# Kernel optimization log

Hardware: AMD Instinct MI355X
Metric: run time of the kernel (lower is better)

Reference implementation:

```python
import jax, jax.numpy as jnp
import numpy as np
import math

D = 3  # feature dim hardcoded in source


def setup_inputs() -> dict:
    key = jax.random.key(0)
    k1, k2, k3, k4 = jax.random.split(key, 4)
    B, H, S = 4, 8, 2048
    x = jax.random.normal(k1, (B, 1, S, D), dtype=jnp.float32)
    W_query = jax.random.normal(k2, (1, H, D, D), dtype=jnp.float32)
    W_key = jax.random.uniform(k3, (1, H, D, D), dtype=jnp.float32)
    W_value = jax.random.uniform(k4, (1, H, D, D), dtype=jnp.float32)
    return {"x": x, "W_query": W_query, "W_key": W_key, "W_value": W_value}


def reference(x, W_query, W_key, W_value):
    # Q/K/V projections: [B,1,S,d] @ [1,H,d,d] -> [B,H,S,d]
    Q = jnp.einsum('bosd,ohde->bhse', x, W_query)
    K = jnp.einsum('bosd,ohde->bhse', x, W_key)
    V = jnp.einsum('bosd,ohde->bhse', x, W_value)
    scale = 1.0 / math.sqrt(D)
    # scores: [B,H,S,S]
    scores = jnp.einsum('bhqd,bhkd->bhqk', Q, K) * scale
    weights = jax.nn.softmax(scores, axis=-1)
    ctx = jnp.einsum('bhqk,bhkd->bhqd', weights, V)
    # source returns (torch result, flash result) — mathematically identical
    return (ctx, ctx)
```

## Files before the change

### kernel.cpp

```cpp
#include <hip/hip_runtime.h>

#define SEQ 2048
#define NH 8
#define NB 4

typedef unsigned int u32;
typedef short bf16x8_t __attribute__((ext_vector_type(8)));
typedef float f32x16_t __attribute__((ext_vector_type(16)));

__device__ __forceinline__ u32 pkb(float a, float b) {
    const u32 ua = __builtin_bit_cast(u32, a) + 0x8000u;
    const u32 ub = __builtin_bit_cast(u32, b) + 0x8000u;
    return __builtin_amdgcn_perm(ub, ua, 0x07060302u);
}
__device__ __forceinline__ u32 pks(float Fa, float Fb) {
    return __builtin_amdgcn_perm(__builtin_bit_cast(u32, Fb),
                                 __builtin_bit_cast(u32, Fa), 0x05040100u);
}

union UBv { bf16x8_t v; u32 u[4]; };

__global__ __launch_bounds__(512)
void attn_mfma(const float* __restrict__ x, const float* __restrict__ Wq,
               const float* __restrict__ Wk, const float* __restrict__ Wv,
               float* __restrict__ out) {
    __shared__ __align__(16) char VT4[128 * 128];
    __shared__ __align__(16) float RED[4][8][8][16];

    const int tid = threadIdx.x;
    const int blk = blockIdx.x;
    const int qb   = blk & 63;
    const int rest = blk >> 6;
    const int hp   = rest & 1;
    const int b    = rest >> 1;
    const int hbase = hp * 4;

    const float* xb = x + b * SEQ * 3;

    const int lane = tid & 63;
    const int wid  = tid >> 6;
    const int ql   = lane & 31;
    const int q    = qb * 32 + ql;
    const int kbase = wid * 256;

    float ax0[8], ax1[8], ax2[8];
#pragma unroll
    for (int t = 0; t < 8; ++t) {
        const float* kp = xb + (kbase + t * 32 + ql) * 3;
        ax0[t] = kp[0]; ax1[t] = kp[1]; ax2[t] = kp[2];
    }

    {
        const float4* xg = (const float4*)xb;
        float xv[12];
        const float4 t0 = xg[tid * 3 + 0]; xv[0]=t0.x; xv[1]=t0.y; xv[2]=t0.z; xv[3]=t0.w;
        const float4 t1 = xg[tid * 3 + 1]; xv[4]=t1.x; xv[5]=t1.y; xv[6]=t1.z; xv[7]=t1.w;
        const float4 t2 = xg[tid * 3 + 2]; xv[8]=t2.x; xv[9]=t2.y; xv[10]=t2.z; xv[11]=t2.w;
        const int k0   = tid * 4;
        const int kt   = k0 >> 4;
        const int run  = k0 & 12;
        const int slotA = (run & 3) | ((run & 4) << 1) | ((run & 8) >> 1);
        char* base = VT4 + kt * 128;
#pragma unroll
        for (int d = 0; d < 3; ++d) {
            uint2 wa;
            wa.x = pkb(xv[0 + d], xv[3 + d]);
            wa.y = pkb(xv[6 + d], xv[9 + d]);
            *(uint2*)(base + d * 32 + slotA * 2) = wa;
        }
        uint2 ones; ones.x = ones.y = 0x3F803F80u;
        *(uint2*)(base + 96 + (k0 & 15) * 2) = ones;
    }

    u32 A0[8], A1h[4];
#pragma unroll
    for (int t = 0; t < 8; ++t) A0[t] = pkb(ax0[t], ax1[t]);
#pragma unroll
    for (int j = 0; j < 4; ++j) A1h[j] = pkb(ax2[2 * j], ax2[2 * j + 1]);

    const float* gq = xb + q * 3;
    const float xq0 = gq[0], xq1 = gq[1], xq2 = gq[2];
    const float cc = 0.5773502691896258f * 1.4426950408889634f * 128.0f;
    float uu[4][3];
#pragma unroll
    for (int hh = 0; hh < 4; ++hh) {
        const float* wqp = Wq + (hbase + hh) * 9;
        const float* wkp = Wk + (hbase + hh) * 9;
        const float Q0 = xq0 * wqp[0] + xq1 * wqp[3] + xq2 * wqp[6];
        const float Q1 = xq0 * wqp[1] + xq1 * wqp[4] + xq2 * wqp[7];
        const float Q2 = xq0 * wqp[2] + xq1 * wqp[5] + xq2 * wqp[8];
        uu[hh][0] = (Q0 * wkp[0] + Q1 * wkp[1] + Q2 * wkp[2]) * cc;
        uu[hh][1] = (Q0 * wkp[3] + Q1 * wkp[4] + Q2 * wkp[5]) * cc;
        uu[hh][2] = (Q0 * wkp[6] + Q1 * wkp[7] + Q2 * wkp[8]) * cc;
    }

    __syncthreads();

    UBv Bs0, Bs1, Bs2, Bs3;
    Bs0.u[0] = (lane < 32) ? pkb(uu[0][0], uu[0][1]) : 0u;
    Bs0.u[1] = (lane < 32) ? pkb(uu[0][2], 0.f) : 0u;
    Bs0.u[2] = 0u; Bs0.u[3] = 0u;
    Bs1.u[0] = (lane < 32) ? pkb(uu[1][0], uu[1][1]) : 0u;
    Bs1.u[1] = (lane < 32) ? pkb(uu[1][2], 0.f) : 0u;
    Bs1.u[2] = 0u; Bs1.u[3] = 0u;
    Bs2.u[0] = (lane < 32) ? pkb(uu[2][0], uu[2][1]) : 0u;
    Bs2.u[1] = (lane < 32) ? pkb(uu[2][2], 0.f) : 0u;
    Bs2.u[2] = 0u; Bs2.u[3] = 0u;
    Bs3.u[0] = (lane < 32) ? pkb(uu[3][0], uu[3][1]) : 0u;
    Bs3.u[1] = (lane < 32) ? pkb(uu[3][2], 0.f) : 0u;
    Bs3.u[2] = 0u; Bs3.u[3] = 0u;

    const char* vb = VT4 + wid * 2048 + (lane & 3) * 32 + (lane >> 5) * 16;

    f32x16_t bc;
#pragma unroll
    for (int i = 0; i < 16; ++i) bc[i] = 8404864.0f;

    const int d31 = lane & 31;
    const int slot = ((lane >> 5) << 2) | d31;

    f32x16_t pv0 = {}, pv1 = {}, pv2 = {}, pv3 = {};

#pragma unroll
    for (int t = 0; t < 8; ++t) {
        const uint4 bv0 = *(const uint4*)(vb + t * 256);
        const uint4 bv1 = *(const uint4*)(vb + t * 256 + 128);
        UBv B0; B0.u[0] = bv0.x; B0.u[1] = bv0.y; B0.u[2] = bv0.z; B0.u[3] = bv0.w;
        UBv B1; B1.u[0] = bv1.x; B1.u[1] = bv1.y; B1.u[2] = bv1.z; B1.u[3] = bv1.w;

        UBv A;
        A.u[0] = A0[t];
        A.u[1] = (t & 1) ? (A1h[t >> 1] >> 16) : (A1h[t >> 1] & 0xFFFFu);
        A.u[2] = 0u; A.u[3] = 0u;

        {
            const f32x16_t sc = __builtin_amdgcn_mfma_f32_32x32x16_bf16(A.v, Bs0.v, bc, 0, 0, 0);
            UBv PA;
            PA.u[0] = pks(sc[0],  sc[1]);  PA.u[1] = pks(sc[2],  sc[3]);
            PA.u[2] = pks(sc[4],  sc[5]);  PA.u[3] = pks(sc[6],  sc[7]);
            pv0 = __builtin_amdgcn_mfma_f32_32x32x16_bf16(PA.v, B0.v, pv0, 0, 0, 0);
            UBv PB;
            PB.u[0] = pks(sc[8],  sc[9]);  PB.u[1] = pks(sc[10], sc[11]);
            PB.u[2] = pks(sc[12], sc[13]); PB.u[3] = pks(sc[14], sc[15]);
            pv0 = __builtin_amdgcn_mfma_f32_32x32x16_bf16(PB.v, B1.v, pv0, 0, 0, 0);
        }
        {
            const f32x16_t sc = __builtin_amdgcn_mfma_f32_32x32x16_bf16(A.v, Bs1.v, bc, 0, 0, 0);
            UBv PA;
            PA.u[0] = pks(sc[0],  sc[1]);  PA.u[1] = pks(sc[2],  sc[3]);
            PA.u[2] = pks(sc[4],  sc[5]);  PA.u[3] = pks(sc[6],  sc[7]);
            pv1 = __builtin_amdgcn_mfma_f32_32x32x16_bf16(PA.v, B0.v, pv1, 0, 0, 0);
            UBv PB;
            PB.u[0] = pks(sc[8],  sc[9]);  PB.u[1] = pks(sc[10], sc[11]);
            PB.u[2] = pks(sc[12], sc[13]); PB.u[3] = pks(sc[14], sc[15]);
            pv1 = __builtin_amdgcn_mfma_f32_32x32x16_bf16(PB.v, B1.v, pv1, 0, 0, 0);
        }
        {
            const f32x16_t sc = __builtin_amdgcn_mfma_f32_32x32x16_bf16(A.v, Bs2.v, bc, 0, 0, 0);
            UBv PA;
            PA.u[0] = pks(sc[0],  sc[1]);  PA.u[1] = pks(sc[2],  sc[3]);
            PA.u[2] = pks(sc[4],  sc[5]);  PA.u[3] = pks(sc[6],  sc[7]);
            pv2 = __builtin_amdgcn_mfma_f32_32x32x16_bf16(PA.v, B0.v, pv2, 0, 0, 0);
            UBv PB;
            PB.u[0] = pks(sc[8],  sc[9]);  PB.u[1] = pks(sc[10], sc[11]);
            PB.u[2] = pks(sc[12], sc[13]); PB.u[3] = pks(sc[14], sc[15]);
            pv2 = __builtin_amdgcn_mfma_f32_32x32x16_bf16(PB.v, B1.v, pv2, 0, 0, 0);
        }
        {
            const f32x16_t sc = __builtin_amdgcn_mfma_f32_32x32x16_bf16(A.v, Bs3.v, bc, 0, 0, 0);
            UBv PA;
            PA.u[0] = pks(sc[0],  sc[1]);  PA.u[1] = pks(sc[2],  sc[3]);
            PA.u[2] = pks(sc[4],  sc[5]);  PA.u[3] = pks(sc[6],  sc[7]);
            pv3 = __builtin_amdgcn_mfma_f32_32x32x16_bf16(PA.v, B0.v, pv3, 0, 0, 0);
            UBv PB;
            PB.u[0] = pks(sc[8],  sc[9]);  PB.u[1] = pks(sc[10], sc[11]);
            PB.u[2] = pks(sc[12], sc[13]); PB.u[3] = pks(sc[14], sc[15]);
            pv3 = __builtin_amdgcn_mfma_f32_32x32x16_bf16(PB.v, B1.v, pv3, 0, 0, 0);
        }
    }

    if (d31 < 4) {
#pragma unroll
        for (int i = 0; i < 4; ++i) {
            float4 w;
            w.x = pv0[i*4+0]; w.y = pv0[i*4+1]; w.z = pv0[i*4+2]; w.w = pv0[i*4+3];
            *(float4*)&RED[0][wid][slot][i * 4] = w;
            w.x = pv1[i*4+0]; w.y = pv1[i*4+1]; w.z = pv1[i*4+2]; w.w = pv1[i*4+3];
            *(float4*)&RED[1][wid][slot][i * 4] = w;
            w.x = pv2[i*4+0]; w.y = pv2[i*4+1]; w.z = pv2[i*4+2]; w.w = pv2[i*4+3];
            *(float4*)&RED[2][wid][slot][i * 4] = w;
            w.x = pv3[i*4+0]; w.y = pv3[i*4+1]; w.z = pv3[i*4+2]; w.w = pv3[i*4+3];
            *(float4*)&RED[3][wid][slot][i * 4] = w;
        }
    }
    __syncthreads();

    if (wid < 4 && lane < 32) {
        const int head = wid;
        const int hh   = hbase + head;
        const float* wvp = Wv + hh * 9;
        const int qrow = lane;
        const int hh2 = (qrow >> 2) & 1;
        const int r   = (qrow & 3) | ((qrow >> 3) << 2);
        float acc[4];
#pragma unroll
        for (int d = 0; d < 4; ++d) {
            float s = 0.f;
#pragma unroll
            for (int w = 0; w < 8; ++w) s += RED[head][w][hh2 * 4 + d][r];
            acc[d] = s;
        }
        const float inv = 1.0f / fmaxf(acc[3], 1e-37f);
        const float r0 = acc[0] * inv, r1 = acc[1] * inv, r2 = acc[2] * inv;
        const float o0 = r0 * wvp[0] + r1 * wvp[3] + r2 * wvp[6];
        const float o1 = r0 * wvp[1] + r1 * wvp[4] + r2 * wvp[7];
        const float o2 = r0 * wvp[2] + r1 * wvp[5] + r2 * wvp[8];
        const int bhO = b * NH + hh;
        const int o   = bhO * (SEQ * 3) + (qb * 32 + qrow) * 3;
        const int second = NB * NH * SEQ * 3;
        out[o + 0] = o0; out[o + 1] = o1; out[o + 2] = o2;
        out[o + second + 0] = o0; out[o + second + 1] = o1; out[o + second + 2] = o2;
    }
}

extern "C" void kernel_launch(void* const* d_in, const int* in_sizes, int n_in,
                              void* d_out, int out_size, void* d_ws, size_t ws_size,
                              hipStream_t stream) {
    const float* x  = (const float*)d_in[0];
    const float* Wq = (const float*)d_in[1];
    const float* Wk = (const float*)d_in[2];
    const float* Wv = (const float*)d_in[3];
    float* out = (float*)d_out;
    (void)in_sizes; (void)n_in; (void)d_ws; (void)ws_size; (void)out_size;

    const int grid = NB * (NH / 4) * (SEQ / 32);
    attn_mfma<<<grid, 512, 0, stream>>>(x, Wq, Wk, Wv, out);
}
```

Baseline: 16.83 us.

## Process all eight heads per block to reuse staged K/V tile

Each block now loops over both groups of four heads instead of handling one group, which halves the grid. The staged x/V tile in shared memory and the per-lane key registers are built once and reused across all eight heads, removing the duplicated staging and launch work. In exchange there are fewer blocks (256 on a large GPU), each block runs longer with an extra barrier per head group, and occupancy and parallelism drop.

```diff
diff --git a/kernel.cpp b/kernel.cpp
--- a/kernel.cpp
+++ b/kernel.cpp
@@ -29,11 +29,8 @@
 
     const int tid = threadIdx.x;
     const int blk = blockIdx.x;
-    const int qb   = blk & 63;
-    const int rest = blk >> 6;
-    const int hp   = rest & 1;
-    const int b    = rest >> 1;
-    const int hbase = hp * 4;
+    const int qb  = blk & 63;
+    const int b   = blk >> 6;
 
     const float* xb = x + b * SEQ * 3;
 
@@ -81,34 +78,22 @@
     const float* gq = xb + q * 3;
     const float xq0 = gq[0], xq1 = gq[1], xq2 = gq[2];
     const float cc = 0.5773502691896258f * 1.4426950408889634f * 128.0f;
-    float uu[4][3];
-#pragma unroll
-    for (int hh = 0; hh < 4; ++hh) {
-        const float* wqp = Wq + (hbase + hh) * 9;
-        const float* wkp = Wk + (hbase + hh) * 9;
+    u32 BsW[8][2];
+#pragma unroll
+    for (int hh = 0; hh < 8; ++hh) {
+        const float* wqp = Wq + hh * 9;
+        const float* wkp = Wk + hh * 9;
         const float Q0 = xq0 * wqp[0] + xq1 * wqp[3] + xq2 * wqp[6];
         const float Q1 = xq0 * wqp[1] + xq1 * wqp[4] + xq2 * wqp[7];
         const float Q2 = xq0 * wqp[2] + xq1 * wqp[5] + xq2 * wqp[8];
-        uu[hh][0] = (Q0 * wkp[0] + Q1 * wkp[1] + Q2 * wkp[2]) * cc;
-        uu[hh][1] = (Q0 * wkp[3] + Q1 * wkp[4] + Q2 * wkp[5]) * cc;
-        uu[hh][2] = (Q0 * wkp[6] + Q1 * wkp[7] + Q2 * wkp[8]) * cc;
+        const float u0 = (Q0 * wkp[0] + Q1 * wkp[1] + Q2 * wkp[2]) * cc;
+        const float u1 = (Q0 * wkp[3] + Q1 * wkp[4] + Q2 * wkp[5]) * cc;
+        const float u2 = (Q0 * wkp[6] + Q1 * wkp[7] + Q2 * wkp[8]) * cc;
+        BsW[hh][0] = (lane < 32) ? pkb(u0, u1) : 0u;
+        BsW[hh][1] = (lane < 32) ? pkb(u2, 0.f) : 0u;
     }
 
     __syncthreads();
-
-    UBv Bs0, Bs1, Bs2, Bs3;
-    Bs0.u[0] = (lane < 32) ? pkb(uu[0][0], uu[0][1]) : 0u;
-    Bs0.u[1] = (lane < 32) ? pkb(uu[0][2], 0.f) : 0u;
-    Bs0.u[2] = 0u; Bs0.u[3] = 0u;
-    Bs1.u[0] = (lane < 32) ? pkb(uu[1][0], uu[1][1]) : 0u;
-    Bs1.u[1] = (lane < 32) ? pkb(uu[1][2], 0.f) : 0u;
-    Bs1.u[2] = 0u; Bs1.u[3] = 0u;
-    Bs2.u[0] = (lane < 32) ? pkb(uu[2][0], uu[2][1]) : 0u;
-    Bs2.u[1] = (lane < 32) ? pkb(uu[2][2], 0.f) : 0u;
-    Bs2.u[2] = 0u; Bs2.u[3] = 0u;
-    Bs3.u[0] = (lane < 32) ? pkb(uu[3][0], uu[3][1]) : 0u;
-    Bs3.u[1] = (lane < 32) ? pkb(uu[3][2], 0.f) : 0u;
-    Bs3.u[2] = 0u; Bs3.u[3] = 0u;
 
     const char* vb = VT4 + wid * 2048 + (lane & 3) * 32 + (lane >> 5) * 16;
 
@@ -118,108 +103,119 @@
 
     const int d31 = lane & 31;
     const int slot = ((lane >> 5) << 2) | d31;
-
-    f32x16_t pv0 = {}, pv1 = {}, pv2 = {}, pv3 = {};
-
-#pragma unroll
-    for (int t = 0; t < 8; ++t) {
-        const uint4 bv0 = *(const uint4*)(vb + t * 256);
-        const uint4 bv1 = *(const uint4*)(vb + t * 256 + 128);
-        UBv B0; B0.u[0] = bv0.x; B0.u[1] = bv0.y; B0.u[2] = bv0.z; B0.u[3] = bv0.w;
-        UBv B1; B1.u[0] = bv1.x; B1.u[1] = bv1.y; B1.u[2] = bv1.z; B1.u[3] = bv1.w;
-
-        UBv A;
-        A.u[0] = A0[t];
-        A.u[1] = (t & 1) ? (A1h[t >> 1] >> 16) : (A1h[t >> 1] & 0xFFFFu);
-        A.u[2] = 0u; A.u[3] = 0u;
-
-        {
-            const f32x16_t sc = __builtin_amdgcn_mfma_f32_32x32x16_bf16(A.v, Bs0.v, bc, 0, 0, 0);
-            UBv PA;
-            PA.u[0] = pks(sc[0],  sc[1]);  PA.u[1] = pks(sc[2],  sc[3]);
-            PA.u[2] = pks(sc[4],  sc[5]);  PA.u[3] = pks(sc[6],  sc[7]);
-            pv0 = __builtin_amdgcn_mfma_f32_32x32x16_bf16(PA.v, B0.v, pv0, 0, 0, 0);
-            UBv PB;
-            PB.u[0] = pks(sc[8],  sc[9]);  PB.u[1] = pks(sc[10], sc[11]);
-            PB.u[2] = pks(sc[12], sc[13]); PB.u[3] = pks(sc[14], sc[15]);
-            pv0 = __builtin_amdgcn_mfma_f32_32x32x16_bf16(PB.v, B1.v, pv0, 0, 0, 0);
-        }
-        {
-            const f32x16_t sc = __builtin_amdgcn_mfma_f32_32x32x16_bf16(A.v, Bs1.v, bc, 0, 0, 0);
-            UBv PA;
-            PA.u[0] = pks(sc[0],  sc[1]);  PA.u[1] = pks(sc[2],  sc[3]);
-            PA.u[2] = pks(sc[4],  sc[5]);  PA.u[3] = pks(sc[6],  sc[7]);
-            pv1 = __builtin_amdgcn_mfma_f32_32x32x16_bf16(PA.v, B0.v, pv1, 0, 0, 0);
-            UBv PB;
-            PB.u[0] = pks(sc[8],  sc[9]);  PB.u[1] = pks(sc[10], sc[11]);
-            PB.u[2] = pks(sc[12], sc[13]); PB.u[3] = pks(sc[14], sc[15]);
-            pv1 = __builtin_amdgcn_mfma_f32_32x32x16_bf16(PB.v, B1.v, pv1, 0, 0, 0);
-        }
-        {
-            const f32x16_t sc = __builtin_amdgcn_mfma_f32_32x32x16_bf16(A.v, Bs2.v, bc, 0, 0, 0);
-            UBv PA;
-            PA.u[0] = pks(sc[0],  sc[1]);  PA.u[1] = pks(sc[2],  sc[3]);
-            PA.u[2] = pks(sc[4],  sc[5]);  PA.u[3] = pks(sc[6],  sc[7]);
-            pv2 = __builtin_amdgcn_mfma_f32_32x32x16_bf16(PA.v, B0.v, pv2, 0, 0, 0);
-            UBv PB;
-            PB.u[0] = pks(sc[8],  sc[9]);  PB.u[1] = pks(sc[10], sc[11]);
-            PB.u[2] = pks(sc[12], sc[13]); PB.u[3] = pks(sc[14], sc[15]);
-            pv2 = __builtin_amdgcn_mfma_f32_32x32x16_bf16(PB.v, B1.v, pv2, 0, 0, 0);
-        }
-        {
-            const f32x16_t sc = __builtin_amdgcn_mfma_f32_32x32x16_bf16(A.v, Bs3.v, bc, 0, 0, 0);
-            UBv PA;
-            PA.u[0] = pks(sc[0],  sc[1]);  PA.u[1] = pks(sc[2],  sc[3]);
-            PA.u[2] = pks(sc[4],  sc[5]);  PA.u[3] = pks(sc[6],  sc[7]);
-            pv3 = __builtin_amdgcn_mfma_f32_32x32x16_bf16(PA.v, B0.v, pv3, 0, 0, 0);
-            UBv PB;
-            PB.u[0] = pks(sc[8],  sc[9]);  PB.u[1] = pks(sc[10], sc[11]);
-            PB.u[2] = pks(sc[12], sc[13]); PB.u[3] = pks(sc[14], sc[15]);
-            pv3 = __builtin_amdgcn_mfma_f32_32x32x16_bf16(PB.v, B1.v, pv3, 0, 0, 0);
-        }
-    }
-
-    if (d31 < 4) {
-#pragma unroll
-        for (int i = 0; i < 4; ++i) {
-            float4 w;
-            w.x = pv0[i*4+0]; w.y = pv0[i*4+1]; w.z = pv0[i*4+2]; w.w = pv0[i*4+3];
-            *(float4*)&RED[0][wid][slot][i * 4] = w;
-            w.x = pv1[i*4+0]; w.y = pv1[i*4+1]; w.z = pv1[i*4+2]; w.w = pv1[i*4+3];
-            *(float4*)&RED[1][wid][slot][i * 4] = w;
-            w.x = pv2[i*4+0]; w.y = pv2[i*4+1]; w.z = pv2[i*4+2]; w.w = pv2[i*4+3];
-            *(float4*)&RED[2][wid][slot][i * 4] = w;
-            w.x = pv3[i*4+0]; w.y = pv3[i*4+1]; w.z = pv3[i*4+2]; w.w = pv3[i*4+3];
-            *(float4*)&RED[3][wid][slot][i * 4] = w;
-        }
-    }
-    __syncthreads();
-
-    if (wid < 4 && lane < 32) {
-        const int head = wid;
-        const int hh   = hbase + head;
-        const float* wvp = Wv + hh * 9;
-        const int qrow = lane;
-        const int hh2 = (qrow >> 2) & 1;
-        const int r   = (qrow & 3) | ((qrow >> 3) << 2);
-        float acc[4];
-#pragma unroll
-        for (int d = 0; d < 4; ++d) {
-            float s = 0.f;
-#pragma unroll
-            for (int w = 0; w < 8; ++w) s += RED[head][w][hh2 * 4 + d][r];
-            acc[d] = s;
-        }
-        const float inv = 1.0f / fmaxf(acc[3], 1e-37f);
-        const float r0 = acc[0] * inv, r1 = acc[1] * inv, r2 = acc[2] * inv;
-        const float o0 = r0 * wvp[0] + r1 * wvp[3] + r2 * wvp[6];
-        const float o1 = r0 * wvp[1] + r1 * wvp[4] + r2 * wvp[7];
-        const float o2 = r0 * wvp[2] + r1 * wvp[5] + r2 * wvp[8];
-        const int bhO = b * NH + hh;
-        const int o   = bhO * (SEQ * 3) + (qb * 32 + qrow) * 3;
-        const int second = NB * NH * SEQ * 3;
-        out[o + 0] = o0; out[o + 1] = o1; out[o + 2] = o2;
-        out[o + second + 0] = o0; out[o + second + 1] = o1; out[o + second + 2] = o2;
+    const int second = NB * NH * SEQ * 3;
+
+#pragma unroll
+    for (int hq = 0; hq < 2; ++hq) {
+        const int hbase = hq * 4;
+        UBv Bs0, Bs1, Bs2, Bs3;
+        Bs0.u[0] = BsW[hbase + 0][0]; Bs0.u[1] = BsW[hbase + 0][1]; Bs0.u[2] = 0u; Bs0.u[3] = 0u;
+        Bs1.u[0] = BsW[hbase + 1][0]; Bs1.u[1] = BsW[hbase + 1][1]; Bs1.u[2] = 0u; Bs1.u[3] = 0u;
+        Bs2.u[0] = BsW[hbase + 2][0]; Bs2.u[1] = BsW[hbase + 2][1]; Bs2.u[2] = 0u; Bs2.u[3] = 0u;
+        Bs3.u[0] = BsW[hbase + 3][0]; Bs3.u[1] = BsW[hbase + 3][1]; Bs3.u[2] = 0u; Bs3.u[3] = 0u;
+
+        f32x16_t pv0 = {}, pv1 = {}, pv2 = {}, pv3 = {};
+
+#pragma unroll
+        for (int t = 0; t < 8; ++t) {
+            const uint4 bv0 = *(const uint4*)(vb + t * 256);
+            const uint4 bv1 = *(const uint4*)(vb + t * 256 + 128);
+            UBv B0; B0.u[0] = bv0.x; B0.u[1] = bv0.y; B0.u[2] = bv0.z; B0.u[3] = bv0.w;
+            UBv B1; B1.u[0] = bv1.x; B1.u[1] = bv1.y; B1.u[2] = bv1.z; B1.u[3] = bv1.w;
+
+            UBv A;
+            A.u[0] = A0[t];
+            A.u[1] = (t & 1) ? (A1h[t >> 1] >> 16) : (A1h[t >> 1] & 0xFFFFu);
+            A.u[2] = 0u; A.u[3] = 0u;
+
+            {
+                const f32x16_t sc = __builtin_amdgcn_mfma_f32_32x32x16_bf16(A.v, Bs0.v, bc, 0, 0, 0);
+                UBv PA;
+                PA.u[0] = pks(sc[0],  sc[1]);  PA.u[1] = pks(sc[2],  sc[3]);
+                PA.u[2] = pks(sc[4],  sc[5]);  PA.u[3] = pks(sc[6],  sc[7]);
+                pv0 = __builtin_amdgcn_mfma_f32_32x32x16_bf16(PA.v, B0.v, pv0, 0, 0, 0);
+                UBv PB;
+                PB.u[0] = pks(sc[8],  sc[9]);  PB.u[1] = pks(sc[10], sc[11]);
+                PB.u[2] = pks(sc[12], sc[13]); PB.u[3] = pks(sc[14], sc[15]);
+                pv0 = __builtin_amdgcn_mfma_f32_32x32x16_bf16(PB.v, B1.v, pv0, 0, 0, 0);
+            }
+            {
+                const f32x16_t sc = __builtin_amdgcn_mfma_f32_32x32x16_bf16(A.v, Bs1.v, bc, 0, 0, 0);
+                UBv PA;
+                PA.u[0] = pks(sc[0],  sc[1]);  PA.u[1] = pks(sc[2],  sc[3]);
+                PA.u[2] = pks(sc[4],  sc[5]);  PA.u[3] = pks(sc[6],  sc[7]);
+                pv1 = __builtin_amdgcn_mfma_f32_32x32x16_bf16(PA.v, B0.v, pv1, 0, 0, 0);
+                UBv PB;
+                PB.u[0] = pks(sc[8],  sc[9]);  PB.u[1] = pks(sc[10], sc[11]);
+                PB.u[2] = pks(sc[12], sc[13]); PB.u[3] = pks(sc[14], sc[15]);
+                pv1 = __builtin_amdgcn_mfma_f32_32x32x16_bf16(PB.v, B1.v, pv1, 0, 0, 0);
+            }
+            {
+                const f32x16_t sc = __builtin_amdgcn_mfma_f32_32x32x16_bf16(A.v, Bs2.v, bc, 0, 0, 0);
+                UBv PA;
+                PA.u[0] = pks(sc[0],  sc[1]);  PA.u[1] = pks(sc[2],  sc[3]);
+                PA.u[2] = pks(sc[4],  sc[5]);  PA.u[3] = pks(sc[6],  sc[7]);
+                pv2 = __builtin_amdgcn_mfma_f32_32x32x16_bf16(PA.v, B0.v, pv2, 0, 0, 0);
+                UBv PB;
+                PB.u[0] = pks(sc[8],  sc[9]);  PB.u[1] = pks(sc[10], sc[11]);
+                PB.u[2] = pks(sc[12], sc[13]); PB.u[3] = pks(sc[14], sc[15]);
+                pv2 = __builtin_amdgcn_mfma_f32_32x32x16_bf16(PB.v, B1.v, pv2, 0, 0, 0);
+            }
+            {
+                const f32x16_t sc = __builtin_amdgcn_mfma_f32_32x32x16_bf16(A.v, Bs3.v, bc, 0, 0, 0);
+                UBv PA;
+                PA.u[0] = pks(sc[0],  sc[1]);  PA.u[1] = pks(sc[2],  sc[3]);
+                PA.u[2] = pks(sc[4],  sc[5]);  PA.u[3] = pks(sc[6],  sc[7]);
+                pv3 = __builtin_amdgcn_mfma_f32_32x32x16_bf16(PA.v, B0.v, pv3, 0, 0, 0);
+                UBv PB;
+                PB.u[0] = pks(sc[8],  sc[9]);  PB.u[1] = pks(sc[10], sc[11]);
+                PB.u[2] = pks(sc[12], sc[13]); PB.u[3] = pks(sc[14], sc[15]);
+                pv3 = __builtin_amdgcn_mfma_f32_32x32x16_bf16(PB.v, B1.v, pv3, 0, 0, 0);
+            }
+        }
+
+        if (d31 < 4) {
+#pragma unroll
+            for (int i = 0; i < 4; ++i) {
+                float4 w;
+                w.x = pv0[i*4+0]; w.y = pv0[i*4+1]; w.z = pv0[i*4+2]; w.w = pv0[i*4+3];
+                *(float4*)&RED[0][wid][slot][i * 4] = w;
+                w.x = pv1[i*4+0]; w.y = pv1[i*4+1]; w.z = pv1[i*4+2]; w.w = pv1[i*4+3];
+                *(float4*)&RED[1][wid][slot][i * 4] = w;
+                w.x = pv2[i*4+0]; w.y = pv2[i*4+1]; w.z = pv2[i*4+2]; w.w = pv2[i*4+3];
+                *(float4*)&RED[2][wid][slot][i * 4] = w;
+                w.x = pv3[i*4+0]; w.y = pv3[i*4+1]; w.z = pv3[i*4+2]; w.w = pv3[i*4+3];
+                *(float4*)&RED[3][wid][slot][i * 4] = w;
+            }
+        }
+        __syncthreads();
+
+        if (wid < 4 && lane < 32) {
+            const int head = wid;
+            const int hh   = hbase + head;
+            const float* wvp = Wv + hh * 9;
+            const int qrow = lane;
+            const int hh2 = (qrow >> 2) & 1;
+            const int r   = (qrow & 3) | ((qrow >> 3) << 2);
+            float acc[4];
+#pragma unroll
+            for (int d = 0; d < 4; ++d) {
+                float s = 0.f;
+#pragma unroll
+                for (int w = 0; w < 8; ++w) s += RED[head][w][hh2 * 4 + d][r];
+                acc[d] = s;
+            }
+            const float inv = 1.0f / fmaxf(acc[3], 1e-37f);
+            const float r0 = acc[0] * inv, r1 = acc[1] * inv, r2 = acc[2] * inv;
+            const float o0 = r0 * wvp[0] + r1 * wvp[3] + r2 * wvp[6];
+            const float o1 = r0 * wvp[1] + r1 * wvp[4] + r2 * wvp[7];
+            const float o2 = r0 * wvp[2] + r1 * wvp[5] + r2 * wvp[8];
+            const int bhO = b * NH + hh;
+            const int o   = bhO * (SEQ * 3) + (qb * 32 + qrow) * 3;
+            out[o + 0] = o0; out[o + 1] = o1; out[o + 2] = o2;
+            out[o + second + 0] = o0; out[o + second + 1] = o1; out[o + second + 2] = o2;
+        }
+        __syncthreads();
     }
 }
 
@@ -233,6 +229,6 @@
     float* out = (float*)d_out;
     (void)in_sizes; (void)n_in; (void)d_ws; (void)ws_size; (void)out_size;
 
-    const int grid = NB * (NH / 4) * (SEQ / 32);
+    const int grid = NB * (SEQ / 32);
     attn_mfma<<<grid, 512, 0, stream>>>(x, Wq, Wk, Wv, out);
 }
```

After: 16.53 us. Within noise of the previous version (-1.8%).
